# Optimization experiments

Measured on AMD Instinct MI355X. Metric: run time of the kernel, lower is better.

The kernel has to match this reference:

```python
import jax, jax.numpy as jnp
import numpy as np

N = 50000        # num nodes == num augmented nodes
E = 800000       # num edges
EMB = 128        # emb_dim
ATTR = 16        # edge_attr_size
L = 3            # num_layers
EPS = 1e-5       # LayerNorm eps


def setup_inputs() -> dict:
    key = jax.random.key(0)
    ks = jax.random.split(key, 11)
    node_feature_view = jax.random.normal(ks[0], (N, EMB), jnp.float32)
    augmented_view = jax.random.normal(ks[1], (N, EMB), jnp.float32)
    edge_index = jax.random.randint(ks[2], (2, E), 0, N, dtype=jnp.int64)
    edge_attr = jax.random.normal(ks[3], (E, ATTR), jnp.float32)
    boundary_condition = jax.random.normal(ks[4], (N, EMB), jnp.float32)
    # per-layer params, stacked on leading layer dim (torch Linear default init range)
    s_m = 1.0 / np.sqrt(EMB + ATTR)
    s_l = 1.0 / np.sqrt(EMB)
    Wm = jax.random.uniform(ks[5], (L, EMB, EMB + ATTR), jnp.float32, -s_m, s_m)
    bm = jax.random.uniform(ks[6], (L, EMB), jnp.float32, -s_m, s_m)
    Wl = jax.random.uniform(ks[7], (L, EMB, EMB), jnp.float32, -s_l, s_l)
    bl = jax.random.uniform(ks[8], (L, EMB), jnp.float32, -s_l, s_l)
    ln_g = jnp.ones((L, EMB), jnp.float32)
    ln_b = jnp.zeros((L, EMB), jnp.float32)
    return dict(node_feature_view=node_feature_view, augmented_view=augmented_view,
                edge_index=edge_index, edge_attr=edge_attr,
                boundary_condition=boundary_condition,
                Wm=Wm, bm=bm, Wl=Wl, bl=bl, ln_g=ln_g, ln_b=ln_b)


def _layer_norm(x, g, b):
    mu = jnp.mean(x, axis=-1, keepdims=True)
    var = jnp.mean(jnp.square(x - mu), axis=-1, keepdims=True)
    return (x - mu) * jax.lax.rsqrt(var + EPS) * g + b


def reference(node_feature_view, augmented_view, edge_index, edge_attr,
              boundary_condition, Wm, bm, Wl, bl, ln_g, ln_b):
    src = edge_index[0]
    dst = edge_index[1]
    # messages depend only on node_feature_view (same gather every layer)
    msg_in = jnp.concatenate([node_feature_view[src], edge_attr], axis=1)  # [E, EMB+ATTR]
    h = augmented_view
    for l in range(L):
        msg = jax.nn.relu(msg_in @ Wm[l].T + bm[l])                        # [E, EMB]
        # scatter-sum edges into augmented nodes; self-loops add boundary_condition
        agg = jax.ops.segment_sum(msg, dst, num_segments=N) + boundary_condition
        out = agg @ Wl[l].T + bl[l]                                        # [N, EMB]
        h = jax.nn.relu(_layer_norm(out, ln_g[l], ln_b[l]))                # dropout: eval mode
    return h
```

## Files before the change

kernel.cpp:

```cpp
#include <hip/hip_runtime.h>

#define NNODES 50000
#define NEDGES 800000
#define EMB    128
#define ATTR   16
#define KIN    144
#define LAYER  2
#define CAP    48
#define NBLK_U 782
#define NBLK_H 782
#define NBLK_T 1

typedef unsigned int uint32;
typedef float v2f __attribute__((ext_vector_type(2)));

__device__ __forceinline__ uint32 pack_bf16(float lo, float hi) {
    uint32 a = __float_as_uint(lo);
    uint32 b = __float_as_uint(hi);
    a += 0x7fffu + ((a >> 16) & 1u);
    b += 0x7fffu + ((b >> 16) & 1u);
    return (a >> 16) | (b & 0xffff0000u);
}

__global__ __launch_bounds__(256) void fused_u_hist(
    const float* __restrict__ x, const float* __restrict__ Wm,
    const float* __restrict__ bm, unsigned short* __restrict__ Ub,
    const int* __restrict__ dst, const int* __restrict__ src,
    int* __restrict__ deg, int2* __restrict__ slab,
    const float* __restrict__ Wl, float4* __restrict__ Wq)
{
    __shared__ float As[EMB * 64];
    __shared__ float Wc[16 * 128];

    if (blockIdx.x >= NBLK_U + NBLK_H) {
        #pragma unroll
        for (int q = 0; q < 16; ++q) {
            const int idx = q * 256 + threadIdx.x;
            const int l = idx & 63, k2 = idx >> 6;
            const float* r0 = Wl + (size_t)(2 * l) * EMB + 2 * k2;
            const float* r1 = r0 + EMB;
            float2 a = *(const float2*)r0;
            float2 c = *(const float2*)r1;
            Wq[idx] = make_float4(a.x, c.x, a.y, c.y);
        }
        return;
    }

    if (blockIdx.x >= NBLK_U) {
        const int e4 = ((blockIdx.x - NBLK_U) * 256 + threadIdx.x) * 4;
        if (e4 < NEDGES) {
            int4 d = *(const int4*)(dst + e4);
            int4 s = *(const int4*)(src + e4);
            int r;
            r = atomicAdd(&deg[d.x], 1);
            if (r < CAP) slab[(size_t)d.x * CAP + r] = make_int2(s.x, e4 + 0);
            r = atomicAdd(&deg[d.y], 1);
            if (r < CAP) slab[(size_t)d.y * CAP + r] = make_int2(s.y, e4 + 1);
            r = atomicAdd(&deg[d.z], 1);
            if (r < CAP) slab[(size_t)d.z * CAP + r] = make_int2(s.z, e4 + 2);
            r = atomicAdd(&deg[d.w], 1);
            if (r < CAP) slab[(size_t)d.w * CAP + r] = make_int2(s.w, e4 + 3);
        }
        return;
    }

    const int t = threadIdx.x, tx = t & 15, ty = t >> 4;
    const int n0 = blockIdx.x * 64;

    {
        const int n = t & 63, qtr = t >> 6;
        const int node = n0 + n;
        const bool ok = node < NNODES;
        const float* xr = x + (size_t)node * EMB;
        #pragma unroll
        for (int q = 0; q < 8; ++q) {
            const int k = qtr * 32 + q * 4;
            float4 v = ok ? *(const float4*)(xr + k) : make_float4(0.f, 0.f, 0.f, 0.f);
            As[(k + 0) * 64 + n] = v.x;
            As[(k + 1) * 64 + n] = v.y;
            As[(k + 2) * 64 + n] = v.z;
            As[(k + 3) * 64 + n] = v.w;
        }
    }

    float acc[4][8];
    #pragma unroll
    for (int i = 0; i < 4; ++i)
        #pragma unroll
        for (int j = 0; j < 8; ++j) acc[i][j] = 0.f;

    for (int kc = 0; kc < 8; ++kc) {
        __syncthreads();
        {
            const int j = t & 127, h = t >> 7;
            const float* wrow = Wm + (size_t)j * KIN + kc * 16 + h * 8;
            float4 v0 = *(const float4*)(wrow);
            float4 v1 = *(const float4*)(wrow + 4);
            Wc[(h * 8 + 0) * 128 + j] = v0.x;
            Wc[(h * 8 + 1) * 128 + j] = v0.y;
            Wc[(h * 8 + 2) * 128 + j] = v0.z;
            Wc[(h * 8 + 3) * 128 + j] = v0.w;
            Wc[(h * 8 + 4) * 128 + j] = v1.x;
            Wc[(h * 8 + 5) * 128 + j] = v1.y;
            Wc[(h * 8 + 6) * 128 + j] = v1.z;
            Wc[(h * 8 + 7) * 128 + j] = v1.w;
        }
        __syncthreads();
        #pragma unroll
        for (int kl = 0; kl < 16; ++kl) {
            const int k = kc * 16 + kl;
            float4 a  = *(const float4*)(As + k * 64 + ty * 4);
            float4 w0 = *(const float4*)(Wc + kl * 128 + tx * 8);
            float4 w1 = *(const float4*)(Wc + kl * 128 + tx * 8 + 4);
            const float av[4] = {a.x, a.y, a.z, a.w};
            const float wv[8] = {w0.x, w0.y, w0.z, w0.w, w1.x, w1.y, w1.z, w1.w};
            #pragma unroll
            for (int i = 0; i < 4; ++i)
                #pragma unroll
                for (int j = 0; j < 8; ++j)
                    acc[i][j] += av[i] * wv[j];
        }
    }

    float bmv[8];
    #pragma unroll
    for (int j = 0; j < 8; ++j) bmv[j] = bm[tx * 8 + j];

    #pragma unroll
    for (int i = 0; i < 4; ++i) {
        const int node = n0 + ty * 4 + i;
        if (node < NNODES) {
            float o[8];
            #pragma unroll
            for (int j = 0; j < 8; ++j) o[j] = acc[i][j] + bmv[j];
            uint4 pk;
            pk.x = pack_bf16(o[0], o[1]);
            pk.y = pack_bf16(o[2], o[3]);
            pk.z = pack_bf16(o[4], o[5]);
            pk.w = pack_bf16(o[6], o[7]);
            *(uint4*)(Ub + (size_t)node * EMB + tx * 8) = pk;
        }
    }
}

__global__ __launch_bounds__(256) void edge_accum_out(
    const unsigned short* __restrict__ Ub, const float* __restrict__ ea,
    const int2* __restrict__ slab, const float* __restrict__ Wm,
    const float* __restrict__ bc, const int* __restrict__ deg,
    const float4* __restrict__ Wq, const float* __restrict__ bl,
    const float* __restrict__ g, const float* __restrict__ b,
    float* __restrict__ out)
{
    __shared__ float ash[4][EMB];

    const int t    = threadIdx.x;
    const int lane = t & 63;
    const int wv   = t >> 6;
    const int node = blockIdx.x * 4 + wv;
    const int c0   = lane * 2;

    v2f w[16];
    {
        const float* wp0 = Wm + (size_t)c0 * KIN + EMB;
        const float* wp1 = wp0 + KIN;
        #pragma unroll
        for (int k = 0; k < 16; k += 4) {
            float4 a = *(const float4*)(wp0 + k);
            float4 bq = *(const float4*)(wp1 + k);
            w[k + 0] = (v2f){a.x, bq.x};
            w[k + 1] = (v2f){a.y, bq.y};
            w[k + 2] = (v2f){a.z, bq.z};
            w[k + 3] = (v2f){a.w, bq.w};
        }
    }

    v2f acc;
    {
        float2 bcv = *(const float2*)(bc + (size_t)node * EMB + c0);
        acc = (v2f){bcv.x, bcv.y};
    }

    int cnt = __builtin_amdgcn_readfirstlane(deg[node]);
    cnt = cnt > CAP ? CAP : cnt;
    const int2* sl = slab + (size_t)node * CAP;

    int i = 0;
    int sa = 0, sb = 0, sc2 = 0, sd = 0, e0 = 0, e1 = 0, e2 = 0, e3 = 0;
    if (0 < cnt) {
        int2 p0 = sl[0], p1 = sl[1], p2 = sl[2], p3 = sl[3];
        sa  = __builtin_amdgcn_readfirstlane(p0.x);
        e0  = __builtin_amdgcn_readfirstlane(p0.y);
        sb  = __builtin_amdgcn_readfirstlane(1 < cnt ? p1.x : 0);
        e1  = __builtin_amdgcn_readfirstlane(1 < cnt ? p1.y : 0);
        sc2 = __builtin_amdgcn_readfirstlane(2 < cnt ? p2.x : 0);
        e2  = __builtin_amdgcn_readfirstlane(2 < cnt ? p2.y : 0);
        sd  = __builtin_amdgcn_readfirstlane(3 < cnt ? p3.x : 0);
        e3  = __builtin_amdgcn_readfirstlane(3 < cnt ? p3.y : 0);
    }

    while (i < cnt) {
        const int rem = cnt - i;

        const uint32 ua = *(const uint32*)(Ub + (size_t)sa  * EMB + c0);
        const uint32 ub = *(const uint32*)(Ub + (size_t)sb  * EMB + c0);
        const uint32 uc = *(const uint32*)(Ub + (size_t)sc2 * EMB + c0);
        const uint32 ud = *(const uint32*)(Ub + (size_t)sd  * EMB + c0);

        const float* p0 = ea + (size_t)e0 * ATTR;
        const float* p1 = ea + (size_t)e1 * ATTR;
        const float* p2 = ea + (size_t)e2 * ATTR;
        const float* p3 = ea + (size_t)e3 * ATTR;
        float4 A0 = *(const float4*)(p0),      A1 = *(const float4*)(p0 + 4);
        float4 A2 = *(const float4*)(p0 + 8),  A3 = *(const float4*)(p0 + 12);
        float4 B0 = *(const float4*)(p1),      B1 = *(const float4*)(p1 + 4);
        float4 B2 = *(const float4*)(p1 + 8),  B3 = *(const float4*)(p1 + 12);
        float4 C0 = *(const float4*)(p2),      C1 = *(const float4*)(p2 + 4);
        float4 C2 = *(const float4*)(p2 + 8),  C3 = *(const float4*)(p2 + 12);
        float4 D0 = *(const float4*)(p3),      D1 = *(const float4*)(p3 + 4);
        float4 D2 = *(const float4*)(p3 + 8),  D3 = *(const float4*)(p3 + 12);

        const int inext = i + 4;
        int nsa = 0, nsb = 0, nsc = 0, nsd = 0, ne0 = 0, ne1 = 0, ne2 = 0, ne3 = 0;
        if (inext < cnt) {
            int2 q0 = sl[inext], q1 = sl[inext + 1], q2 = sl[inext + 2], q3 = sl[inext + 3];
            nsa = __builtin_amdgcn_readfirstlane(q0.x);
            ne0 = __builtin_amdgcn_readfirstlane(q0.y);
            nsb = __builtin_amdgcn_readfirstlane(inext + 1 < cnt ? q1.x : 0);
            ne1 = __builtin_amdgcn_readfirstlane(inext + 1 < cnt ? q1.y : 0);
            nsc = __builtin_amdgcn_readfirstlane(inext + 2 < cnt ? q2.x : 0);
            ne2 = __builtin_amdgcn_readfirstlane(inext + 2 < cnt ? q2.y : 0);
            nsd = __builtin_amdgcn_readfirstlane(inext + 3 < cnt ? q3.x : 0);
            ne3 = __builtin_amdgcn_readfirstlane(inext + 3 < cnt ? q3.y : 0);
        }

        #define DOT16(V0, V1, V2, V3, m)                                        \
            do {                                                                \
                m  = V0.x * w[0];  m += V0.y * w[1];                            \
                m += V0.z * w[2];  m += V0.w * w[3];                            \
                m += V1.x * w[4];  m += V1.y * w[5];                            \
                m += V1.z * w[6];  m += V1.w * w[7];                            \
                m += V2.x * w[8];  m += V2.y * w[9];                            \
                m += V2.z * w[10]; m += V2.w * w[11];                           \
                m += V3.x * w[12]; m += V3.y * w[13];                           \
                m += V3.z * w[14]; m += V3.w * w[15];                           \
            } while (0)

        v2f m;
        DOT16(A0, A1, A2, A3, m);
        m += (v2f){__uint_as_float(ua << 16), __uint_as_float(ua & 0xffff0000u)};
        m.x = fmaxf(m.x, 0.f); m.y = fmaxf(m.y, 0.f);
        acc += m;

        DOT16(B0, B1, B2, B3, m);
        m += (v2f){__uint_as_float(ub << 16), __uint_as_float(ub & 0xffff0000u)};
        m.x = fmaxf(m.x, 0.f); m.y = fmaxf(m.y, 0.f);
        if (rem > 1) acc += m;

        DOT16(C0, C1, C2, C3, m);
        m += (v2f){__uint_as_float(uc << 16), __uint_as_float(uc & 0xffff0000u)};
        m.x = fmaxf(m.x, 0.f); m.y = fmaxf(m.y, 0.f);
        if (rem > 2) acc += m;

        DOT16(D0, D1, D2, D3, m);
        m += (v2f){__uint_as_float(ud << 16), __uint_as_float(ud & 0xffff0000u)};
        m.x = fmaxf(m.x, 0.f); m.y = fmaxf(m.y, 0.f);
        if (rem > 3) acc += m;
        #undef DOT16

        sa = nsa; sb = nsb; sc2 = nsc; sd = nsd;
        e0 = ne0; e1 = ne1; e2 = ne2; e3 = ne3;
        i = inext;
    }

    *(float2*)&ash[wv][c0] = make_float2(acc.x, acc.y);
    __syncthreads();

    v2f o = (v2f){0.f, 0.f};
    #pragma unroll 2
    for (int kc = 0; kc < 8; ++kc) {
        float4 a0 = *(const float4*)&ash[wv][kc * 16 + 0];
        float4 a1 = *(const float4*)&ash[wv][kc * 16 + 4];
        float4 a2 = *(const float4*)&ash[wv][kc * 16 + 8];
        float4 a3 = *(const float4*)&ash[wv][kc * 16 + 12];
        const float4* qp = Wq + (size_t)(kc * 8) * 64 + lane;
        float4 q0 = qp[0 * 64], q1 = qp[1 * 64], q2 = qp[2 * 64], q3 = qp[3 * 64];
        float4 q4 = qp[4 * 64], q5 = qp[5 * 64], q6 = qp[6 * 64], q7 = qp[7 * 64];
        o += a0.x * (v2f){q0.x, q0.y}; o += a0.y * (v2f){q0.z, q0.w};
        o += a0.z * (v2f){q1.x, q1.y}; o += a0.w * (v2f){q1.z, q1.w};
        o += a1.x * (v2f){q2.x, q2.y}; o += a1.y * (v2f){q2.z, q2.w};
        o += a1.z * (v2f){q3.x, q3.y}; o += a1.w * (v2f){q3.z, q3.w};
        o += a2.x * (v2f){q4.x, q4.y}; o += a2.y * (v2f){q4.z, q4.w};
        o += a2.z * (v2f){q5.x, q5.y}; o += a2.w * (v2f){q5.z, q5.w};
        o += a3.x * (v2f){q6.x, q6.y}; o += a3.y * (v2f){q6.z, q6.w};
        o += a3.z * (v2f){q7.x, q7.y}; o += a3.w * (v2f){q7.z, q7.w};
    }

    float2 blv = *(const float2*)(bl + c0);
    const float u0 = o.x + blv.x;
    const float u1 = o.y + blv.y;
    float s = u0 + u1, s2 = u0 * u0 + u1 * u1;
    #pragma unroll
    for (int off = 1; off < 64; off <<= 1) {
        s  += __shfl_xor(s, off, 64);
        s2 += __shfl_xor(s2, off, 64);
    }
    const float mu   = s * (1.f / 128.f);
    const float var  = s2 * (1.f / 128.f) - mu * mu;
    const float rstd = rsqrtf(var + 1e-5f);
    float2 gv2 = *(const float2*)(g + c0);
    float2 bv2 = *(const float2*)(b + c0);
    float r0 = (u0 - mu) * rstd * gv2.x + bv2.x;
    float r1 = (u1 - mu) * rstd * gv2.y + bv2.y;
    r0 = r0 > 0.f ? r0 : 0.f;
    r1 = r1 > 0.f ? r1 : 0.f;
    *(float2*)(out + (size_t)node * EMB + c0) = make_float2(r0, r1);
}

extern "C" void kernel_launch(void* const* d_in, const int* in_sizes, int n_in,
                              void* d_out, int out_size, void* d_ws, size_t ws_size,
                              hipStream_t stream) {
    const float* x  = (const float*)d_in[0];
    const int*   ei = (const int*)d_in[2];
    const float* ea = (const float*)d_in[3];
    const float* bc = (const float*)d_in[4];
    const float* Wm = (const float*)d_in[5];
    const float* bm = (const float*)d_in[6];
    const float* Wl = (const float*)d_in[7];
    const float* bl = (const float*)d_in[8];
    const float* g  = (const float*)d_in[9];
    const float* b  = (const float*)d_in[10];
    float* out = (float*)d_out;

    const int* src = ei;
    const int* dst = ei + NEDGES;

    int* deg = (int*)d_ws;
    size_t off_s = (((size_t)NNODES * sizeof(int)) + 255) & ~(size_t)255;
    int2* slab = (int2*)((char*)d_ws + off_s);
    size_t off_u = (off_s + (size_t)NNODES * CAP * sizeof(int2) + 255) & ~(size_t)255;
    unsigned short* Ub = (unsigned short*)((char*)d_ws + off_u);
    size_t off_q = (off_u + (size_t)NNODES * EMB * sizeof(unsigned short) + 255) & ~(size_t)255;
    float4* Wq = (float4*)((char*)d_ws + off_q);

    const float* WmL = Wm + (size_t)LAYER * EMB * KIN;
    const float* WlL = Wl + (size_t)LAYER * EMB * EMB;

    hipMemsetAsync(deg, 0, (size_t)NNODES * sizeof(int), stream);

    fused_u_hist<<<NBLK_U + NBLK_H + NBLK_T, 256, 0, stream>>>(
        x, WmL, bm + LAYER * EMB, Ub, dst, src, deg, slab, WlL, Wq);

    edge_accum_out<<<NNODES / 4, 256, 0, stream>>>(
        Ub, ea, slab, WmL, bc, deg, Wq, bl + LAYER * EMB,
        g + LAYER * EMB, b + LAYER * EMB, out);
}
```

Measured before the change: 401.0 us.

## Prefetch edge data one iteration ahead and split output GEMV across waves

The edge loop now loads the whole adjacency slab into lanes once and pulls indices out with readlane, so no scalar loads sit in the loop. It also issues the gathers for the next group of 4 edges before computing the current group, a software pipeline meant to hide gather latency. The output linear layer is repartitioned so each wave computes a column slice for all 4 nodes, reading a bf16-packed aggregate from shared memory. This cuts redundant Wq loads per wave, at the cost of an extra barrier for the cross-wave LayerNorm reduction, more registers, and bf16 rounding of the aggregate.

```diff
diff --git a/kernel.cpp b/kernel.cpp
--- a/kernel.cpp
+++ b/kernel.cpp
@@ -36,8 +36,8 @@
         #pragma unroll
         for (int q = 0; q < 16; ++q) {
             const int idx = q * 256 + threadIdx.x;
-            const int l = idx & 63, k2 = idx >> 6;
-            const float* r0 = Wl + (size_t)(2 * l) * EMB + 2 * k2;
+            const int cp = idx & 63, k2 = idx >> 6;
+            const float* r0 = Wl + (size_t)(2 * cp) * EMB + 2 * k2;
             const float* r1 = r0 + EMB;
             float2 a = *(const float2*)r0;
             float2 c = *(const float2*)r1;
@@ -151,13 +151,19 @@
     const float* __restrict__ g, const float* __restrict__ b,
     float* __restrict__ out)
 {
-    __shared__ float ash[4][EMB];
+    __shared__ uint32 aggL[4][64];
+    __shared__ float2 red[4][4];
 
     const int t    = threadIdx.x;
     const int lane = t & 63;
     const int wv   = t >> 6;
     const int node = blockIdx.x * 4 + wv;
     const int c0   = lane * 2;
+
+    const int2* sl = slab + (size_t)node * CAP;
+    const int2 sv  = sl[lane < CAP ? lane : CAP - 1];
+    const int  dv  = deg[node];
+    const float2 bcv = *(const float2*)(bc + (size_t)node * EMB + c0);
 
     v2f w[16];
     {
@@ -174,64 +180,66 @@
         }
     }
 
-    v2f acc;
-    {
-        float2 bcv = *(const float2*)(bc + (size_t)node * EMB + c0);
-        acc = (v2f){bcv.x, bcv.y};
-    }
-
-    int cnt = __builtin_amdgcn_readfirstlane(deg[node]);
+    int cnt = __builtin_amdgcn_readfirstlane(dv);
     cnt = cnt > CAP ? CAP : cnt;
-    const int2* sl = slab + (size_t)node * CAP;
+
+    v2f acc = (v2f){bcv.x, bcv.y};
+
+    #define SLOT(j, S, E)                                               \
+        do {                                                            \
+            const int jj_ = (j);                                        \
+            const int s_ = __builtin_amdgcn_readlane(sv.x, jj_ & 63);   \
+            const int e_ = __builtin_amdgcn_readlane(sv.y, jj_ & 63);   \
+            S = jj_ < cnt ? s_ : 0;                                     \
+            E = jj_ < cnt ? e_ : 0;                                     \
+        } while (0)
+
+    int sa, sb, sc2, sd, e0, e1, e2, e3;
+    SLOT(0, sa, e0); SLOT(1, sb, e1); SLOT(2, sc2, e2); SLOT(3, sd, e3);
+
+    uint32 ua = *(const uint32*)(Ub + (size_t)sa  * EMB + c0);
+    uint32 ub = *(const uint32*)(Ub + (size_t)sb  * EMB + c0);
+    uint32 uc = *(const uint32*)(Ub + (size_t)sc2 * EMB + c0);
+    uint32 ud = *(const uint32*)(Ub + (size_t)sd  * EMB + c0);
+
+    const float* p0 = ea + (size_t)e0 * ATTR;
+    const float* p1 = ea + (size_t)e1 * ATTR;
+    const float* p2 = ea + (size_t)e2 * ATTR;
+    const float* p3 = ea + (size_t)e3 * ATTR;
+    float4 A0 = *(const float4*)(p0),      A1 = *(const float4*)(p0 + 4);
+    float4 A2 = *(const float4*)(p0 + 8),  A3 = *(const float4*)(p0 + 12);
+    float4 B0 = *(const float4*)(p1),      B1 = *(const float4*)(p1 + 4);
+    float4 B2 = *(const float4*)(p1 + 8),  B3 = *(const float4*)(p1 + 12);
+    float4 C0 = *(const float4*)(p2),      C1 = *(const float4*)(p2 + 4);
+    float4 C2 = *(const float4*)(p2 + 8),  C3 = *(const float4*)(p2 + 12);
+    float4 D0 = *(const float4*)(p3),      D1 = *(const float4*)(p3 + 4);
+    float4 D2 = *(const float4*)(p3 + 8),  D3 = *(const float4*)(p3 + 12);
 
     int i = 0;
-    int sa = 0, sb = 0, sc2 = 0, sd = 0, e0 = 0, e1 = 0, e2 = 0, e3 = 0;
-    if (0 < cnt) {
-        int2 p0 = sl[0], p1 = sl[1], p2 = sl[2], p3 = sl[3];
-        sa  = __builtin_amdgcn_readfirstlane(p0.x);
-        e0  = __builtin_amdgcn_readfirstlane(p0.y);
-        sb  = __builtin_amdgcn_readfirstlane(1 < cnt ? p1.x : 0);
-        e1  = __builtin_amdgcn_readfirstlane(1 < cnt ? p1.y : 0);
-        sc2 = __builtin_amdgcn_readfirstlane(2 < cnt ? p2.x : 0);
-        e2  = __builtin_amdgcn_readfirstlane(2 < cnt ? p2.y : 0);
-        sd  = __builtin_amdgcn_readfirstlane(3 < cnt ? p3.x : 0);
-        e3  = __builtin_amdgcn_readfirstlane(3 < cnt ? p3.y : 0);
-    }
-
     while (i < cnt) {
         const int rem = cnt - i;
 
-        const uint32 ua = *(const uint32*)(Ub + (size_t)sa  * EMB + c0);
-        const uint32 ub = *(const uint32*)(Ub + (size_t)sb  * EMB + c0);
-        const uint32 uc = *(const uint32*)(Ub + (size_t)sc2 * EMB + c0);
-        const uint32 ud = *(const uint32*)(Ub + (size_t)sd  * EMB + c0);
-
-        const float* p0 = ea + (size_t)e0 * ATTR;
-        const float* p1 = ea + (size_t)e1 * ATTR;
-        const float* p2 = ea + (size_t)e2 * ATTR;
-        const float* p3 = ea + (size_t)e3 * ATTR;
-        float4 A0 = *(const float4*)(p0),      A1 = *(const float4*)(p0 + 4);
-        float4 A2 = *(const float4*)(p0 + 8),  A3 = *(const float4*)(p0 + 12);
-        float4 B0 = *(const float4*)(p1),      B1 = *(const float4*)(p1 + 4);
-        float4 B2 = *(const float4*)(p1 + 8),  B3 = *(const float4*)(p1 + 12);
-        float4 C0 = *(const float4*)(p2),      C1 = *(const float4*)(p2 + 4);
-        float4 C2 = *(const float4*)(p2 + 8),  C3 = *(const float4*)(p2 + 12);
-        float4 D0 = *(const float4*)(p3),      D1 = *(const float4*)(p3 + 4);
-        float4 D2 = *(const float4*)(p3 + 8),  D3 = *(const float4*)(p3 + 12);
-
-        const int inext = i + 4;
-        int nsa = 0, nsb = 0, nsc = 0, nsd = 0, ne0 = 0, ne1 = 0, ne2 = 0, ne3 = 0;
-        if (inext < cnt) {
-            int2 q0 = sl[inext], q1 = sl[inext + 1], q2 = sl[inext + 2], q3 = sl[inext + 3];
-            nsa = __builtin_amdgcn_readfirstlane(q0.x);
-            ne0 = __builtin_amdgcn_readfirstlane(q0.y);
-            nsb = __builtin_amdgcn_readfirstlane(inext + 1 < cnt ? q1.x : 0);
-            ne1 = __builtin_amdgcn_readfirstlane(inext + 1 < cnt ? q1.y : 0);
-            nsc = __builtin_amdgcn_readfirstlane(inext + 2 < cnt ? q2.x : 0);
-            ne2 = __builtin_amdgcn_readfirstlane(inext + 2 < cnt ? q2.y : 0);
-            nsd = __builtin_amdgcn_readfirstlane(inext + 3 < cnt ? q3.x : 0);
-            ne3 = __builtin_amdgcn_readfirstlane(inext + 3 < cnt ? q3.y : 0);
-        }
+        int nsa, nsb, nsc, nsd, ne0, ne1, ne2, ne3;
+        SLOT(i + 4, nsa, ne0); SLOT(i + 5, nsb, ne1);
+        SLOT(i + 6, nsc, ne2); SLOT(i + 7, nsd, ne3);
+
+        const uint32 nua = *(const uint32*)(Ub + (size_t)nsa * EMB + c0);
+        const uint32 nub = *(const uint32*)(Ub + (size_t)nsb * EMB + c0);
+        const uint32 nuc = *(const uint32*)(Ub + (size_t)nsc * EMB + c0);
+        const uint32 nud = *(const uint32*)(Ub + (size_t)nsd * EMB + c0);
+
+        const float* q0 = ea + (size_t)ne0 * ATTR;
+        const float* q1 = ea + (size_t)ne1 * ATTR;
+        const float* q2 = ea + (size_t)ne2 * ATTR;
+        const float* q3 = ea + (size_t)ne3 * ATTR;
+        float4 NA0 = *(const float4*)(q0),      NA1 = *(const float4*)(q0 + 4);
+        float4 NA2 = *(const float4*)(q0 + 8),  NA3 = *(const float4*)(q0 + 12);
+        float4 NB0 = *(const float4*)(q1),      NB1 = *(const float4*)(q1 + 4);
+        float4 NB2 = *(const float4*)(q1 + 8),  NB3 = *(const float4*)(q1 + 12);
+        float4 NC0 = *(const float4*)(q2),      NC1 = *(const float4*)(q2 + 4);
+        float4 NC2 = *(const float4*)(q2 + 8),  NC3 = *(const float4*)(q2 + 12);
+        float4 ND0 = *(const float4*)(q3),      ND1 = *(const float4*)(q3 + 4);
+        float4 ND2 = *(const float4*)(q3 + 8),  ND3 = *(const float4*)(q3 + 12);
 
         #define DOT16(V0, V1, V2, V3, m)                                        \
             do {                                                                \
@@ -267,53 +275,66 @@
         if (rem > 3) acc += m;
         #undef DOT16
 
-        sa = nsa; sb = nsb; sc2 = nsc; sd = nsd;
-        e0 = ne0; e1 = ne1; e2 = ne2; e3 = ne3;
-        i = inext;
-    }
-
-    *(float2*)&ash[wv][c0] = make_float2(acc.x, acc.y);
+        A0 = NA0; A1 = NA1; A2 = NA2; A3 = NA3;
+        B0 = NB0; B1 = NB1; B2 = NB2; B3 = NB3;
+        C0 = NC0; C1 = NC1; C2 = NC2; C3 = NC3;
+        D0 = ND0; D1 = ND1; D2 = ND2; D3 = ND3;
+        ua = nua; ub = nub; uc = nuc; ud = nud;
+        i += 4;
+    }
+    #undef SLOT
+
+    aggL[wv][lane] = pack_bf16(acc.x, acc.y);
     __syncthreads();
 
+    const int nd = lane >> 4;
+    const int cp = wv * 16 + (lane & 15);
+    const int cc = cp * 2;
+    const float2 blv = *(const float2*)(bl + cc);
+    const float2 gv2 = *(const float2*)(g + cc);
+    const float2 bv2 = *(const float2*)(b + cc);
+
     v2f o = (v2f){0.f, 0.f};
-    #pragma unroll 2
-    for (int kc = 0; kc < 8; ++kc) {
-        float4 a0 = *(const float4*)&ash[wv][kc * 16 + 0];
-        float4 a1 = *(const float4*)&ash[wv][kc * 16 + 4];
-        float4 a2 = *(const float4*)&ash[wv][kc * 16 + 8];
-        float4 a3 = *(const float4*)&ash[wv][kc * 16 + 12];
-        const float4* qp = Wq + (size_t)(kc * 8) * 64 + lane;
+    #pragma unroll
+    for (int k8 = 0; k8 < 8; ++k8) {
+        uint4 a0 = *(const uint4*)&aggL[nd][k8 * 8];
+        uint4 a1 = *(const uint4*)&aggL[nd][k8 * 8 + 4];
+        const float4* qp = Wq + (size_t)(k8 * 8) * 64 + cp;
         float4 q0 = qp[0 * 64], q1 = qp[1 * 64], q2 = qp[2 * 64], q3 = qp[3 * 64];
         float4 q4 = qp[4 * 64], q5 = qp[5 * 64], q6 = qp[6 * 64], q7 = qp[7 * 64];
-        o += a0.x * (v2f){q0.x, q0.y}; o += a0.y * (v2f){q0.z, q0.w};
-        o += a0.z * (v2f){q1.x, q1.y}; o += a0.w * (v2f){q1.z, q1.w};
-        o += a1.x * (v2f){q2.x, q2.y}; o += a1.y * (v2f){q2.z, q2.w};
-        o += a1.z * (v2f){q3.x, q3.y}; o += a1.w * (v2f){q3.z, q3.w};
-        o += a2.x * (v2f){q4.x, q4.y}; o += a2.y * (v2f){q4.z, q4.w};
-        o += a2.z * (v2f){q5.x, q5.y}; o += a2.w * (v2f){q5.z, q5.w};
-        o += a3.x * (v2f){q6.x, q6.y}; o += a3.y * (v2f){q6.z, q6.w};
-        o += a3.z * (v2f){q7.x, q7.y}; o += a3.w * (v2f){q7.z, q7.w};
-    }
-
-    float2 blv = *(const float2*)(bl + c0);
+        #define ACC2(AU, Q)                                                        \
+            do {                                                                   \
+                o += __uint_as_float((AU) << 16)         * (v2f){(Q).x, (Q).y};    \
+                o += __uint_as_float((AU) & 0xffff0000u) * (v2f){(Q).z, (Q).w};    \
+            } while (0)
+        ACC2(a0.x, q0); ACC2(a0.y, q1); ACC2(a0.z, q2); ACC2(a0.w, q3);
+        ACC2(a1.x, q4); ACC2(a1.y, q5); ACC2(a1.z, q6); ACC2(a1.w, q7);
+        #undef ACC2
+    }
+
     const float u0 = o.x + blv.x;
     const float u1 = o.y + blv.y;
     float s = u0 + u1, s2 = u0 * u0 + u1 * u1;
     #pragma unroll
-    for (int off = 1; off < 64; off <<= 1) {
+    for (int off = 1; off < 16; off <<= 1) {
         s  += __shfl_xor(s, off, 64);
         s2 += __shfl_xor(s2, off, 64);
     }
-    const float mu   = s * (1.f / 128.f);
-    const float var  = s2 * (1.f / 128.f) - mu * mu;
+    if ((lane & 15) == 0) red[wv][nd] = make_float2(s, s2);
+    __syncthreads();
+
+    const float2 r0 = red[0][nd], r1 = red[1][nd], r2 = red[2][nd], r3 = red[3][nd];
+    const float s_tot  = r0.x + r1.x + r2.x + r3.x;
+    const float s2_tot = r0.y + r1.y + r2.y + r3.y;
+    const float mu   = s_tot * (1.f / 128.f);
+    const float var  = s2_tot * (1.f / 128.f) - mu * mu;
     const float rstd = rsqrtf(var + 1e-5f);
-    float2 gv2 = *(const float2*)(g + c0);
-    float2 bv2 = *(const float2*)(b + c0);
-    float r0 = (u0 - mu) * rstd * gv2.x + bv2.x;
-    float r1 = (u1 - mu) * rstd * gv2.y + bv2.y;
-    r0 = r0 > 0.f ? r0 : 0.f;
-    r1 = r1 > 0.f ? r1 : 0.f;
-    *(float2*)(out + (size_t)node * EMB + c0) = make_float2(r0, r1);
+
+    float o0 = (u0 - mu) * rstd * gv2.x + bv2.x;
+    float o1 = (u1 - mu) * rstd * gv2.y + bv2.y;
+    o0 = o0 > 0.f ? o0 : 0.f;
+    o1 = o1 > 0.f ? o1 : 0.f;
+    *(float2*)(out + (size_t)(blockIdx.x * 4 + nd) * EMB + cc) = make_float2(o0, o1);
 }
 
 extern "C" void kernel_launch(void* const* d_in, const int* in_sizes, int n_in,
```

Result: faster. 384.1 us (-4.2%).
